# Kernel optimization log

Measured on AMD Instinct MI355X. Metric: run time of the kernel, lower is better.

The kernel has to match this reference:

```python
import jax, jax.numpy as jnp
import numpy as np

E, N, D, DFF, NE = 8, 4096, 1024, 2048, 65536

def setup_inputs() -> dict:
    key = jax.random.key(0)
    k1, k2, k3, k4 = jax.random.split(key, 4)
    x = jax.random.normal(k1, (E, N, D), dtype=jnp.float32)
    W1 = jax.random.normal(k2, (E, D, DFF), dtype=jnp.float32) * (1.0 / np.sqrt(D))
    W2 = jax.random.normal(k3, (E, DFF, D), dtype=jnp.float32) * (1.0 / np.sqrt(DFF))
    edge_index = jax.random.randint(k4, (2, NE), 0, N, dtype=jnp.int64)
    return {"x": x, "W1": W1, "W2": W2, "edge_index": edge_index}

def reference(x, W1, W2, edge_index):
    # Vectorized form of the per-expert Python loop + stack:
    # each expert: h = relu(x_e @ W1_e); agg[dst] += h[src]; out_e = agg @ W2_e
    n = x.shape[1]
    src, dst = edge_index[0], edge_index[1]
    h = jax.nn.relu(jnp.einsum('end,edf->enf', x, W1))  # [e, n, dff]
    msgs = h[:, src, :]                                  # [e, n_edges, dff] (irregular gather)
    agg = jax.vmap(lambda m: jax.ops.segment_sum(m, dst, num_segments=n))(msgs)  # [e, n, dff]
    out = jnp.einsum('enf,efd->end', agg, W2)            # [e, n, d] == x.shape
    return out
```

## Files before the change

kernel.cpp:

```cpp
#include <hip/hip_runtime.h>

#define E_ 8
#define N_ 4096
#define D_ 1024
#define DFF_ 2048
#define NE_ 65536

typedef __attribute__((ext_vector_type(8))) short short8;
typedef __attribute__((ext_vector_type(4))) float f32x4;

__device__ __forceinline__ unsigned short f2bf(float f) {
  unsigned u = __float_as_uint(f);
  u += 0x7fffu + ((u >> 16) & 1u);
  return (unsigned short)(u >> 16);
}
__device__ __forceinline__ float bf2f(unsigned short h) {
  return __uint_as_float(((unsigned)h) << 16);
}


__global__ __launch_bounds__(256) void cvt_f32_bf16_vec(
    const float* __restrict__ in, unsigned short* __restrict__ out, int n4) {
  int i = blockIdx.x * 256 + threadIdx.x;
  if (i >= n4) return;
  float4 v = ((const float4*)in)[i];
  ushort4 o;
  o.x = f2bf(v.x); o.y = f2bf(v.y); o.z = f2bf(v.z); o.w = f2bf(v.w);
  ((ushort4*)out)[i] = o;
}

__global__ __launch_bounds__(256) void transpose_cvt(
    const float* __restrict__ in, unsigned short* __restrict__ out, int R, int C) {
  __shared__ float tile[32][33];
  const int e = blockIdx.z;
  const float* ine = in + (size_t)e * R * C;
  unsigned short* oute = out + (size_t)e * R * C;
  const int c0 = blockIdx.x * 32, r0 = blockIdx.y * 32;
  const int tx = threadIdx.x & 31, ty = threadIdx.x >> 5;
#pragma unroll
  for (int i = 0; i < 32; i += 8)
    tile[ty + i][tx] = ine[(size_t)(r0 + ty + i) * C + (c0 + tx)];
  __syncthreads();
#pragma unroll
  for (int i = 0; i < 32; i += 8)
    oute[(size_t)(c0 + ty + i) * R + (r0 + tx)] = f2bf(tile[tx][ty + i]);
}


__global__ __launch_bounds__(256) void zero_i32(int* __restrict__ p, int n) {
  int i = blockIdx.x * 256 + threadIdx.x;
  if (i < n) p[i] = 0;
}

__global__ __launch_bounds__(256) void hist_dst(
    const int* __restrict__ ei, int* __restrict__ cnt, int ne) {
  int i = blockIdx.x * 256 + threadIdx.x;
  if (i < ne) atomicAdd(&cnt[ei[ne + i]], 1);
}

__global__ __launch_bounds__(1024) void scan4096(
    const int* __restrict__ cnt, int* __restrict__ rowptr, int* __restrict__ cursor) {
  __shared__ int tmp[1024];
  const int tid = threadIdx.x;
  const int b = tid * 4;
  int c0 = cnt[b + 0], c1 = cnt[b + 1], c2 = cnt[b + 2], c3 = cnt[b + 3];
  int tot = c0 + c1 + c2 + c3;
  tmp[tid] = tot;
  __syncthreads();
  int val = tot;
  for (int off = 1; off < 1024; off <<= 1) {
    int v = 0;
    if (tid >= off) v = tmp[tid - off];
    __syncthreads();
    val += v;
    tmp[tid] = val;
    __syncthreads();
  }
  const int excl = val - tot;
  rowptr[b + 0] = excl;
  rowptr[b + 1] = excl + c0;
  rowptr[b + 2] = excl + c0 + c1;
  rowptr[b + 3] = excl + c0 + c1 + c2;
  cursor[b + 0] = excl;
  cursor[b + 1] = excl + c0;
  cursor[b + 2] = excl + c0 + c1;
  cursor[b + 3] = excl + c0 + c1 + c2;
  if (tid == 1023) rowptr[N_] = val;
}

__global__ __launch_bounds__(256) void fill_csr(
    const int* __restrict__ ei, int* __restrict__ cursor, int* __restrict__ csr, int ne) {
  int i = blockIdx.x * 256 + threadIdx.x;
  if (i < ne) {
    int s = ei[i];
    int d = ei[ne + i];
    int pos = atomicAdd(&cursor[d], 1);
    csr[pos] = s;
  }
}


#define BAR() asm volatile("s_barrier" ::: "memory")
#define WAIT_VM(n) asm volatile("s_waitcnt vmcnt(" #n ")" ::: "memory")

template <bool RELU>
__global__ __launch_bounds__(512, 1) void gemm256(
    const unsigned short* __restrict__ A, const unsigned short* __restrict__ BT,
    unsigned short* __restrict__ Cb, int M, int Nm, int K, int nbx, int nbxy) {
  __shared__ char lds[131072];

  const int orig = blockIdx.x;
  const int sw = (orig & 7) * nbxy + (orig >> 3);
  const int e = sw / nbxy;
  const int rem = sw - e * nbxy;
  const int by = rem / nbx;
  const int bx = rem - by * nbx;
  const int m0 = by * 256, n0 = bx * 256;

  const int tid = threadIdx.x;
  const int lane = tid & 63;
  const int wid = tid >> 6;
  const int wm = wid >> 2;
  const int wn = wid & 3;
  const int lo = lane & 15, hi = lane >> 4;

  const unsigned short* Ae = A + (size_t)e * M * K + (size_t)m0 * K;
  const unsigned short* Be = BT + (size_t)e * Nm * K + (size_t)n0 * K;
  unsigned short* Ce = Cb + (size_t)e * M * Nm;

  auto srcoff = [&](int p) -> size_t {
    int R = p >> 3, s = p & 7;
    int bc = s ^ (R & 7);
    int gr = 2 * R + (bc >> 2), c = bc & 3;
    return (size_t)gr * K + (size_t)c * 8;
  };
  const size_t so0 = srcoff(tid);
  const size_t so1 = srcoff(tid + 512);

#define GLD(src_, dst_)                                                        \
  __builtin_amdgcn_global_load_lds(                                            \
      (const __attribute__((address_space(1))) void*)(src_),                   \
      (__attribute__((address_space(3))) void*)(dst_), 16, 0, 0)

#define STAGE(t_)                                                              \
  do {                                                                         \
    char* Lb_ = lds + ((t_) & 3) * 32768;                                      \
    const unsigned short* ga_ = Ae + (size_t)(t_) * 32;                        \
    const unsigned short* gb_ = Be + (size_t)(t_) * 32;                        \
    GLD(ga_ + so0, Lb_ + tid * 16);                                            \
    GLD(ga_ + so1, Lb_ + 8192 + tid * 16);                                     \
    GLD(gb_ + so0, Lb_ + 16384 + tid * 16);                                    \
    GLD(gb_ + so1, Lb_ + 24576 + tid * 16);                                    \
  } while (0)

  const int slot = (((lo & 1) << 2) | hi) ^ ((lo >> 1) & 7);
  const int aoff = (wm * 64 + (lo >> 1)) * 128 + slot * 16;
  const int boff = 16384 + (wn * 32 + (lo >> 1)) * 128 + slot * 16;

  f32x4 acc[8][4];
#pragma unroll
  for (int i = 0; i < 8; ++i)
#pragma unroll
    for (int j = 0; j < 4; ++j) acc[i][j] = (f32x4){0.f, 0.f, 0.f, 0.f};

  short8 afA[8], bfA[4], afB[8], bfB[4];

  auto dsread = [&](short8* af, short8* bfv, int t) {
    const char* L = lds + (t & 3) * 32768;
#pragma unroll
    for (int fm = 0; fm < 8; ++fm) af[fm] = *(const short8*)(L + aoff + fm * 1024);
#pragma unroll
    for (int fn = 0; fn < 4; ++fn) bfv[fn] = *(const short8*)(L + boff + fn * 1024);
  };
  auto domfma = [&](const short8* af, const short8* bfv) {
    __builtin_amdgcn_s_setprio(1);
#pragma unroll
    for (int fm = 0; fm < 8; ++fm)
#pragma unroll
      for (int fn = 0; fn < 4; ++fn)
        acc[fm][fn] = __builtin_amdgcn_mfma_f32_16x16x32_bf16(af[fm], bfv[fn],
                                                              acc[fm][fn], 0, 0, 0);
    __builtin_amdgcn_s_setprio(0);
  };

  const int nkt = K >> 5;

  STAGE(0);
  STAGE(1);
  STAGE(2);
  WAIT_VM(8);
  BAR();
  dsread(afA, bfA, 0);

  int t = 0;
  for (; t + 1 < nkt - 2; t += 2) {
    WAIT_VM(4);
    BAR();
    dsread(afB, bfB, t + 1);
    if (t + 3 < nkt) STAGE(t + 3);
    domfma(afA, bfA);

    WAIT_VM(4);
    BAR();
    dsread(afA, bfA, t + 2);
    if (t + 4 < nkt) STAGE(t + 4);
    domfma(afB, bfB);
  }
  WAIT_VM(0);
  BAR();
  dsread(afB, bfB, nkt - 1);
  domfma(afA, bfA);
  domfma(afB, bfB);

  const int row0 = m0 + wm * 128 + hi * 4;
  const int col0 = n0 + wn * 64 + lo;
#pragma unroll
  for (int fm = 0; fm < 8; ++fm)
#pragma unroll
    for (int fn = 0; fn < 4; ++fn)
#pragma unroll
      for (int r = 0; r < 4; ++r) {
        float v = acc[fm][fn][r];
        if (RELU) v = fmaxf(v, 0.f);
        Ce[(size_t)(row0 + fm * 16 + r) * Nm + (col0 + fn * 16)] = f2bf(v);
      }
#undef STAGE
#undef GLD
}


__global__ __launch_bounds__(256) void gather_sum(
    const unsigned short* __restrict__ y, const int* __restrict__ rowptr,
    const int* __restrict__ csr, float* __restrict__ out) {
  const int dst = blockIdx.x;
  const int e = blockIdx.y;
  const unsigned short* ye = y + (size_t)e * N_ * D_;
  float* oute = out + (size_t)e * N_ * D_ + (size_t)dst * D_;
  const int t = threadIdx.x;
  const int beg = rowptr[dst], end = rowptr[dst + 1];
  float a0 = 0.f, a1 = 0.f, a2 = 0.f, a3 = 0.f;
  for (int i = beg; i < end; ++i) {
    const int s = csr[i];
    ushort4 v = ((const ushort4*)(ye + (size_t)s * D_))[t];
    a0 += bf2f(v.x);
    a1 += bf2f(v.y);
    a2 += bf2f(v.z);
    a3 += bf2f(v.w);
  }
  float4 o;
  o.x = a0; o.y = a1; o.z = a2; o.w = a3;
  ((float4*)oute)[t] = o;
}


extern "C" void kernel_launch(void* const* d_in, const int* in_sizes, int n_in,
                              void* d_out, int out_size, void* d_ws, size_t ws_size,
                              hipStream_t stream) {
  (void)in_sizes; (void)n_in; (void)out_size; (void)ws_size;
  const float* x = (const float*)d_in[0];
  const float* W1 = (const float*)d_in[1];
  const float* W2 = (const float*)d_in[2];
  const int* ei = (const int*)d_in[3];
  float* out = (float*)d_out;

  char* p = (char*)d_ws;
  auto alloc = [&](size_t b) {
    char* r = p;
    p += (b + 255) & ~(size_t)255;
    return r;
  };
  unsigned short* xbf = (unsigned short*)alloc((size_t)E_ * N_ * D_ * 2);
  unsigned short* w1t = (unsigned short*)alloc((size_t)E_ * D_ * DFF_ * 2);
  unsigned short* w2t = (unsigned short*)alloc((size_t)E_ * DFF_ * D_ * 2);
  unsigned short* h = (unsigned short*)alloc((size_t)E_ * N_ * DFF_ * 2);
  unsigned short* y = (unsigned short*)alloc((size_t)E_ * N_ * D_ * 2);
  int* cnt = (int*)alloc((size_t)N_ * 4);
  int* rowptr = (int*)alloc((size_t)(N_ + 1) * 4);
  int* cursor = (int*)alloc((size_t)N_ * 4);
  int* csr = (int*)alloc((size_t)NE_ * 4);

  cvt_f32_bf16_vec<<<(E_ * N_ * D_ / 4 + 255) / 256, 256, 0, stream>>>(x, xbf, E_ * N_ * D_ / 4);
  transpose_cvt<<<dim3(DFF_ / 32, D_ / 32, E_), 256, 0, stream>>>(W1, w1t, D_, DFF_);
  transpose_cvt<<<dim3(D_ / 32, DFF_ / 32, E_), 256, 0, stream>>>(W2, w2t, DFF_, D_);

  zero_i32<<<(N_ + 255) / 256, 256, 0, stream>>>(cnt, N_);
  hist_dst<<<NE_ / 256, 256, 0, stream>>>(ei, cnt, NE_);
  scan4096<<<1, 1024, 0, stream>>>(cnt, rowptr, cursor);
  fill_csr<<<NE_ / 256, 256, 0, stream>>>(ei, cursor, csr, NE_);

  {
    int nbx = DFF_ / 256, nby = N_ / 256;
    gemm256<true><<<nbx * nby * E_, 512, 0, stream>>>(xbf, w1t, h, N_, DFF_, D_, nbx, nbx * nby);
  }
  {
    int nbx = D_ / 256, nby = N_ / 256;
    gemm256<false><<<nbx * nby * E_, 512, 0, stream>>>(h, w2t, y, N_, D_, DFF_, nbx, nbx * nby);
  }

  gather_sum<<<dim3(N_, E_), 256, 0, stream>>>(y, rowptr, csr, out);
}
```

Before: 493.3 us.

## Split gather_sum rows in half, swizzle block order per XCD, unroll edges, nontemporal stores

```diff
diff --git a/kernel.cpp b/kernel.cpp
--- a/kernel.cpp
+++ b/kernel.cpp
@@ -229,27 +229,36 @@
 }
 
 
-__global__ __launch_bounds__(256) void gather_sum(
+__global__ __launch_bounds__(128) void gather_sum(
     const unsigned short* __restrict__ y, const int* __restrict__ rowptr,
     const int* __restrict__ csr, float* __restrict__ out) {
-  const int dst = blockIdx.x;
-  const int e = blockIdx.y;
-  const unsigned short* ye = y + (size_t)e * N_ * D_;
-  float* oute = out + (size_t)e * N_ * D_ + (size_t)dst * D_;
+  const int orig = blockIdx.x;
+  const int sw = (orig & 7) * (E_ * N_ * 2 / 8) + (orig >> 3);
+  const int e = sw >> 13;
+  const int half = (sw >> 12) & 1;
+  const int dst = sw & 4095;
+  const unsigned short* ye = y + (size_t)e * N_ * D_ + half * (D_ / 2);
+  float* oute = out + (size_t)e * N_ * D_ + (size_t)dst * D_ + half * (D_ / 2);
   const int t = threadIdx.x;
   const int beg = rowptr[dst], end = rowptr[dst + 1];
   float a0 = 0.f, a1 = 0.f, a2 = 0.f, a3 = 0.f;
-  for (int i = beg; i < end; ++i) {
+  int i = beg;
+  for (; i + 1 < end; i += 2) {
+    const int s0 = csr[i], s1 = csr[i + 1];
+    ushort4 v0 = ((const ushort4*)(ye + (size_t)s0 * D_))[t];
+    ushort4 v1 = ((const ushort4*)(ye + (size_t)s1 * D_))[t];
+    a0 += bf2f(v0.x) + bf2f(v1.x);
+    a1 += bf2f(v0.y) + bf2f(v1.y);
+    a2 += bf2f(v0.z) + bf2f(v1.z);
+    a3 += bf2f(v0.w) + bf2f(v1.w);
+  }
+  if (i < end) {
     const int s = csr[i];
     ushort4 v = ((const ushort4*)(ye + (size_t)s * D_))[t];
-    a0 += bf2f(v.x);
-    a1 += bf2f(v.y);
-    a2 += bf2f(v.z);
-    a3 += bf2f(v.w);
-  }
-  float4 o;
-  o.x = a0; o.y = a1; o.z = a2; o.w = a3;
-  ((float4*)oute)[t] = o;
+    a0 += bf2f(v.x); a1 += bf2f(v.y); a2 += bf2f(v.z); a3 += bf2f(v.w);
+  }
+  f32x4 o = (f32x4){a0, a1, a2, a3};
+  __builtin_nontemporal_store(o, (f32x4*)oute + t);
 }
 
 
@@ -297,5 +306,5 @@
     gemm256<false><<<nbx * nby * E_, 512, 0, stream>>>(h, w2t, y, N_, D_, DFF_, nbx, nbx * nby);
   }
 
-  gather_sum<<<dim3(N_, E_), 256, 0, stream>>>(y, rowptr, csr, out);
-}
+  gather_sum<<<E_ * N_ * 2, 128, 0, stream>>>(y, rowptr, csr, out);
+}
```

Result: faster. 450.7 us (-8.6%).
